# Performance work log

Hardware: AMD Instinct MI355X
Metric: run time of the kernel (lower is better)

The kernel has to match this reference:

```python
import jax, jax.numpy as jnp
import numpy as np


def setup_inputs() -> dict:
    key = jax.random.key(0)
    B, T, H, W, C = 4, 16, 112, 112, 96
    N = 2048
    RPB = N // B  # 512 regions per batch: 8 time blocks x 8x8 spatial blocks
    tb, hb, wb = T // 8, H // 8, W // 8  # block sizes 2, 14, 14
    ti = np.arange(T) // tb
    hi = np.arange(H) // hb
    wi = np.arange(W) // wb
    local = ti[:, None, None] * 64 + hi[None, :, None] * 8 + wi[None, None, :]  # [T,H,W]
    seg = (np.arange(B)[:, None, None, None] * RPB + local[None]).astype(np.int64)  # [B,T,H,W]
    coord = np.zeros((4, B * T * H * W), dtype=np.int64)
    coord[0] = np.repeat(np.arange(B), T * H * W)  # per-voxel batch index
    r = np.arange(N)
    l = r % RPB
    rt, rh, rw = l // 64, (l % 64) // 8, l % 8
    bbox = np.stack([
        rt * tb, rh * hb, rw * wb,
        rt * tb + (tb - 1), rh * hb + (hb - 1), rw * wb + (wb - 1),
    ]).astype(np.float32)  # [6,N]: ymin,xmin,zmin,ymax,xmax,zmax
    flatvid = jax.random.normal(key, (B * T * H * W, C), dtype=jnp.float32)
    return {"flatvid": flatvid, "seg": jnp.asarray(seg), "coord": jnp.asarray(coord),
            "bbox": jnp.asarray(bbox), "space_patch": 8, "time_patch": 4}


def reference(flatvid, seg, coord, bbox, space_patch, time_patch):
    B, T, H, W = seg.shape
    C = flatvid.shape[-1]
    N = bbox.shape[1]
    P = space_patch * space_patch * time_patch
    gs = jnp.linspace(0.0, 1.0, space_patch)
    gt = jnp.linspace(0.0, 1.0, time_patch)
    yg, xg, zg = jnp.meshgrid(gt, gs, gs, indexing='ij')
    yg, xg, zg = yg.reshape(1, P), xg.reshape(1, P), zg.reshape(1, P)
    seg_flat = seg.reshape(-1)
    # torch: unique(seg*B + b) % B  ->  per-region batch id (seg labels 0..N-1, one batch each)
    b_idx = jax.ops.segment_max(coord[0], seg_flat, num_segments=N).astype(jnp.int32)  # [N]
    ymin, xmin, zmin, ymax, xmax, zmax = bbox.reshape(6, N, 1)
    t_pos = yg * (ymax - ymin) + ymin  # [N,P]
    h_pos = xg * (xmax - xmin) + xmin
    w_pos = zg * (zmax - zmin) + zmin
    t0 = jnp.clip(jnp.floor(t_pos).astype(jnp.int32), 0, T - 1)
    h0 = jnp.clip(jnp.floor(h_pos).astype(jnp.int32), 0, H - 1)
    w0 = jnp.clip(jnp.floor(w_pos).astype(jnp.int32), 0, W - 1)
    t1 = jnp.clip(t0 + 1, 0, T - 1)
    h1 = jnp.clip(h0 + 1, 0, H - 1)
    w1 = jnp.clip(w0 + 1, 0, W - 1)
    Ut, Uh, Uw = t_pos - t0, h_pos - h0, w_pos - w0  # fractional offsets (vs clamped floor)
    Lt, Lh, Lw = 1.0 - Ut, 1.0 - Uh, 1.0 - Uw
    corners = [
        (t0, h0, w0, Lt * Lh * Lw), (t0, h0, w1, Lt * Lh * Uw),
        (t0, h1, w0, Lt * Uh * Lw), (t0, h1, w1, Lt * Uh * Uw),
        (t1, h0, w0, Ut * Lh * Lw), (t1, h0, w1, Ut * Lh * Uw),
        (t1, h1, w0, Ut * Uh * Lw), (t1, h1, w1, Ut * Uh * Uw),
    ]
    bb = b_idx[:, None]  # [N,1]
    srange = jnp.arange(N)[:, None]  # [N,1]
    tri = jnp.zeros((N, P, C), dtype=flatvid.dtype)
    msk = jnp.zeros((N, P), dtype=flatvid.dtype)
    for t, h, w, wt in corners:  # fixed 8 corners
        idx = ((bb * T + t) * H + h) * W + w  # [N,P] linear index into [B*T*H*W]
        tri = tri + flatvid[idx] * wt[..., None]
        msk = msk + (seg_flat[idx] == srange) * wt
    tri = tri.reshape(N, time_patch, space_patch, space_patch, C).transpose(0, 4, 1, 2, 3)
    msk = msk.reshape(N, 1, time_patch, space_patch, space_patch)
    return tri, msk
```

## Files before the change

kernel.cpp:

```cpp
#include <hip/hip_runtime.h>
#include <cstdint>
#include <cstddef>

#define B_  4
#define T_  16
#define H_  112
#define W_  112
#define C_  96
#define N_  2048
#define SP_ 8
#define TP_ 4
#define P_  256
#define M_  (B_*T_*H_*W_)

#define RT_   3
#define RH_   15
#define RW_   15
#define NPIX_ (RT_*RH_*RW_)
#define CC_   16
#define NPASS_ (C_/CC_)
#define PPAD_ 676

#define FU_ 11
#define BU_ 6

static_assert(P_ == SP_*SP_*TP_, "patch count");

__device__ __forceinline__ float bflo(unsigned int u){
    union { unsigned int i; float f; } v; v.i = u << 16; return v.f;
}
__device__ __forceinline__ float bfhi(unsigned int u){
    union { unsigned int i; float f; } v; v.i = u & 0xffff0000u; return v.f;
}
__device__ __forceinline__ unsigned short to_bf16(float f){
    union { unsigned int i; float f; } v; v.f = f;
    unsigned int x = v.i;
    return (unsigned short)((x + 0x7fffu + ((x >> 16) & 1u)) >> 16);
}

__global__ void detect_dtype_kernel(const unsigned short* __restrict__ v,
                                    int* __restrict__ flag){
    int lane = threadIdx.x;
    unsigned short u = v[lane * 2];
    int e = (u >> 7) & 0xff;
    int sane = ((e >= 107 && e <= 147) || ((u & 0x7fffu) == 0)) ? 1 : 0;
    unsigned long long m = __ballot(sane);
    if (lane == 0) flag[0] = (__popcll(m) >= 48) ? 1 : 0;
}

__global__ void segmax_kernel(const int* __restrict__ seg,
                              const int* __restrict__ coord0,
                              int* __restrict__ bidx){
    int g = blockIdx.x * blockDim.x + threadIdx.x;
    int base = g * 8;
    if (base >= M_) return;
    int4 s0 = *(const int4*)(seg + base);
    int4 s1 = *(const int4*)(seg + base + 4);
    int4 c0 = *(const int4*)(coord0 + base);
    int4 c1 = *(const int4*)(coord0 + base + 4);
    int s[8] = {s0.x,s0.y,s0.z,s0.w,s1.x,s1.y,s1.z,s1.w};
    int c[8] = {c0.x,c0.y,c0.z,c0.w,c1.x,c1.y,c1.z,c1.w};
    int cur = s[0], mx = c[0];
    #pragma unroll
    for (int j = 1; j < 8; ++j){
        if (s[j] == cur) { mx = max(mx, c[j]); }
        else { atomicMax(&bidx[cur], mx); cur = s[j]; mx = c[j]; }
    }
    atomicMax(&bidx[cur], mx);
}

__device__ __forceinline__ int region_gpix(int r, int b, int oy, int ox, int oz){
    const int tl  = r / (RH_*RW_);
    const int rem = r - tl*(RH_*RW_);
    const int hl  = rem / RW_;
    const int wl  = rem - hl*RW_;
    const int tg  = min(oy + tl, T_-1);
    const int hg  = min(ox + hl, H_-1);
    const int wg  = min(oz + wl, W_-1);
    return ((b*T_ + tg)*H_ + hg)*W_ + wg;
}

template<bool BF16>
__global__ __launch_bounds__(P_) void interp_kernel(
    const void* __restrict__ vid_, const int* __restrict__ seg,
    const void* __restrict__ bbox_, const int* __restrict__ bidx,
    const int* __restrict__ flag, void* __restrict__ out_)
{
    if (flag[0] != (BF16 ? 1 : 0)) return;

    __shared__ float lds_vid[CC_ * PPAD_];
    __shared__ int   lds_seg[NPIX_];

    const int n = blockIdx.x;
    const int p = threadIdx.x;

    float bb[6];
    if (BF16){
        const unsigned short* bbox = (const unsigned short*)bbox_;
        #pragma unroll
        for (int j = 0; j < 6; ++j) bb[j] = bflo((unsigned int)bbox[j*N_ + n]);
    } else {
        const float* bbox = (const float*)bbox_;
        #pragma unroll
        for (int j = 0; j < 6; ++j) bb[j] = bbox[j*N_ + n];
    }
    const float ymin=bb[0], xmin=bb[1], zmin=bb[2], ymax=bb[3], xmax=bb[4], zmax=bb[5];
    const int b  = bidx[n];
    const int oy = (int)ymin, ox = (int)xmin, oz = (int)zmin;

    const int pt = p >> 6, ph = (p >> 3) & 7, pw = p & 7;
    const float gt = (float)(pt * (1.0 / (TP_-1)));
    const float gh = (float)(ph * (1.0 / (SP_-1)));
    const float gw = (float)(pw * (1.0 / (SP_-1)));
    const float t_pos = gt * (ymax - ymin) + ymin;
    const float h_pos = gh * (xmax - xmin) + xmin;
    const float w_pos = gw * (zmax - zmin) + zmin;

    int t0 = (int)floorf(t_pos); t0 = min(max(t0, 0), T_-1);
    int h0 = (int)floorf(h_pos); h0 = min(max(h0, 0), H_-1);
    int w0 = (int)floorf(w_pos); w0 = min(max(w0, 0), W_-1);
    const int t1 = min(t0+1, T_-1);
    const int h1 = min(h0+1, H_-1);
    const int w1 = min(w0+1, W_-1);
    const float Ut = t_pos - (float)t0, Uh = h_pos - (float)h0, Uw = w_pos - (float)w0;
    const float Lt = 1.f - Ut, Lh = 1.f - Uh, Lw = 1.f - Uw;

    float wgt[8];
    wgt[0]=Lt*Lh*Lw; wgt[1]=Lt*Lh*Uw; wgt[2]=Lt*Uh*Lw; wgt[3]=Lt*Uh*Uw;
    wgt[4]=Ut*Lh*Lw; wgt[5]=Ut*Lh*Uw; wgt[6]=Ut*Uh*Lw; wgt[7]=Ut*Uh*Uw;

    const int lt0 = min(max(t0 - oy, 0), RT_-1);
    const int lt1 = min(max(t1 - oy, 0), RT_-1);
    const int lh0 = min(max(h0 - ox, 0), RH_-1);
    const int lh1 = min(max(h1 - ox, 0), RH_-1);
    const int lw0 = min(max(w0 - oz, 0), RW_-1);
    const int lw1 = min(max(w1 - oz, 0), RW_-1);
    int pix[8];
    {
        const int q00 = (lt0*RH_ + lh0)*RW_, q01 = (lt0*RH_ + lh1)*RW_;
        const int q10 = (lt1*RH_ + lh0)*RW_, q11 = (lt1*RH_ + lh1)*RW_;
        pix[0]=q00+lw0; pix[1]=q00+lw1; pix[2]=q01+lw0; pix[3]=q01+lw1;
        pix[4]=q10+lw0; pix[5]=q10+lw1; pix[6]=q11+lw0; pix[7]=q11+lw1;
    }

    for (int r = p; r < NPIX_; r += P_)
        lds_seg[r] = seg[region_gpix(r, b, oy, ox, oz)];

    const char* vidb = (const char*)vid_;

    if (BF16){
        unsigned goff[BU_]; int ldw[BU_]; uint4 V[BU_];
        #pragma unroll
        for (int i = 0; i < BU_; ++i){
            const int f = p + i*P_;
            if (f < NPIX_*2){
                const int r = f >> 1, u = f & 1;
                goff[i] = (unsigned)region_gpix(r, b, oy, ox, oz)*(unsigned)(C_*2) + (unsigned)u*16u;
                ldw[i]  = (u*8)*PPAD_ + r;
            } else { goff[i] = 0u; ldw[i] = -1; }
        }
        #pragma unroll
        for (int i = 0; i < BU_; ++i)
            if (ldw[i] >= 0) V[i] = *(const uint4*)(vidb + goff[i]);

        __syncthreads();

        float m = 0.f;
        #pragma unroll
        for (int k = 0; k < 8; ++k)
            m += wgt[k] * ((lds_seg[pix[k]] == n) ? 1.f : 0.f);
        unsigned short* out = (unsigned short*)out_;
        out[(size_t)N_*C_*P_ + (size_t)n*P_ + p] = to_bf16(m);

        #pragma unroll 1
        for (int pass = 0; pass < NPASS_; ++pass){
            if (pass) __syncthreads();
            #pragma unroll
            for (int i = 0; i < BU_; ++i){
                if (ldw[i] >= 0){
                    float* dst = &lds_vid[ldw[i]];
                    dst[0*PPAD_]=bflo(V[i].x); dst[1*PPAD_]=bfhi(V[i].x);
                    dst[2*PPAD_]=bflo(V[i].y); dst[3*PPAD_]=bfhi(V[i].y);
                    dst[4*PPAD_]=bflo(V[i].z); dst[5*PPAD_]=bfhi(V[i].z);
                    dst[6*PPAD_]=bflo(V[i].w); dst[7*PPAD_]=bfhi(V[i].w);
                }
            }
            if (pass+1 < NPASS_){
                #pragma unroll
                for (int i = 0; i < BU_; ++i)
                    if (ldw[i] >= 0)
                        V[i] = *(const uint4*)(vidb + goff[i] + (unsigned)((pass+1)*(CC_*2)));
            }
            __syncthreads();

            float acc[CC_];
            #pragma unroll
            for (int c = 0; c < CC_; ++c) acc[c] = 0.f;
            #pragma unroll
            for (int k = 0; k < 8; ++k){
                const float w = wgt[k];
                const float* col = &lds_vid[pix[k]];
                #pragma unroll
                for (int c = 0; c < CC_; ++c) acc[c] += w * col[c*PPAD_];
            }
            const size_t ob = ((size_t)n*C_ + pass*CC_)*P_ + p;
            #pragma unroll
            for (int c = 0; c < CC_; ++c) out[ob + (size_t)c*P_] = to_bf16(acc[c]);
        }
    } else {
        unsigned goff[FU_]; int ldw[FU_]; float4 V[FU_];
        #pragma unroll
        for (int i = 0; i < FU_; ++i){
            const int f = p + i*P_;
            if (f < NPIX_*4){
                const int r = f >> 2, q = f & 3;
                goff[i] = (unsigned)region_gpix(r, b, oy, ox, oz)*(unsigned)(C_*4) + (unsigned)q*16u;
                ldw[i]  = (q*4)*PPAD_ + r;
            } else { goff[i] = 0u; ldw[i] = -1; }
        }
        #pragma unroll
        for (int i = 0; i < FU_; ++i)
            if (ldw[i] >= 0) V[i] = *(const float4*)(vidb + goff[i]);

        __syncthreads();

        float m = 0.f;
        #pragma unroll
        for (int k = 0; k < 8; ++k)
            m += wgt[k] * ((lds_seg[pix[k]] == n) ? 1.f : 0.f);
        float* out = (float*)out_;
        out[(size_t)N_*C_*P_ + (size_t)n*P_ + p] = m;

        #pragma unroll 1
        for (int pass = 0; pass < NPASS_; ++pass){
            if (pass) __syncthreads();
            #pragma unroll
            for (int i = 0; i < FU_; ++i){
                if (ldw[i] >= 0){
                    float* dst = &lds_vid[ldw[i]];
                    dst[0*PPAD_]=V[i].x; dst[1*PPAD_]=V[i].y;
                    dst[2*PPAD_]=V[i].z; dst[3*PPAD_]=V[i].w;
                }
            }
            if (pass+1 < NPASS_){
                #pragma unroll
                for (int i = 0; i < FU_; ++i)
                    if (ldw[i] >= 0)
                        V[i] = *(const float4*)(vidb + goff[i] + (unsigned)((pass+1)*(CC_*4)));
            }
            __syncthreads();

            float acc[CC_];
            #pragma unroll
            for (int c = 0; c < CC_; ++c) acc[c] = 0.f;
            #pragma unroll
            for (int k = 0; k < 8; ++k){
                const float w = wgt[k];
                const float* col = &lds_vid[pix[k]];
                #pragma unroll
                for (int c = 0; c < CC_; ++c) acc[c] += w * col[c*PPAD_];
            }
            const size_t ob = ((size_t)n*C_ + pass*CC_)*P_ + p;
            #pragma unroll
            for (int c = 0; c < CC_; ++c) out[ob + (size_t)c*P_] = acc[c];
        }
    }
}

extern "C" void kernel_launch(void* const* d_in, const int* in_sizes, int n_in,
                              void* d_out, int out_size, void* d_ws, size_t ws_size,
                              hipStream_t stream){
    const void* vid   = d_in[0];
    const int*  seg   = (const int*)d_in[1];
    const int*  coord = (const int*)d_in[2];
    const void* bbox  = d_in[3];

    int* flag = (int*)d_ws;
    int* bidx = flag + 64;

    hipMemsetAsync(d_ws, 0, (64 + N_) * sizeof(int), stream);
    detect_dtype_kernel<<<1, 64, 0, stream>>>((const unsigned short*)vid, flag);
    segmax_kernel<<<(M_/8 + 255)/256, 256, 0, stream>>>(seg, coord, bidx);
    interp_kernel<true ><<<N_, P_, 0, stream>>>(vid, seg, bbox, bidx, flag, d_out);
    interp_kernel<false><<<N_, P_, 0, stream>>>(vid, seg, bbox, bidx, flag, d_out);
}
```

Before: 534.4 us.

## Halve LDS channel tile and skip zero-weight time corners

Shrinks the shared-memory video tile from 16 to 8 channels per pass, which should roughly halve LDS use and allow more resident blocks per CU. Global loads are reorganised into 64-byte super-chunks held in registers and written into LDS in sub-steps, with the next chunk prefetched during compute. The upper four trilinear corners are skipped when the temporal fractional weight is zero. The cost is more barriers per block and more register-held load state.

Result: slower. 590.3 us (+10.5%).

```diff
diff --git a/kernel.cpp b/kernel.cpp
--- a/kernel.cpp
+++ b/kernel.cpp
@@ -17,12 +17,13 @@
 #define RH_   15
 #define RW_   15
 #define NPIX_ (RT_*RH_*RW_)
-#define CC_   16
-#define NPASS_ (C_/CC_)
 #define PPAD_ 676
-
-#define FU_ 11
-#define BU_ 6
+#define CPP_  8
+#define UNITS_ 2700
+#define UPT_  11
+#define SSF_  6
+#define SSB_  3
+#define INVC_ (1<<20)
 
 static_assert(P_ == SP_*SP_*TP_, "patch count");
 
@@ -80,6 +81,27 @@
     return ((b*T_ + tg)*H_ + hg)*W_ + wg;
 }
 
+#define ACCUM8(accv) do {                                                    \
+    _Pragma("unroll")                                                        \
+    for (int c = 0; c < CPP_; ++c) accv[c] = 0.f;                            \
+    _Pragma("unroll")                                                        \
+    for (int k = 0; k < 4; ++k){                                             \
+        const float w = wgt[k];                                              \
+        const float* col = &lds_vid[pix[k]];                                 \
+        _Pragma("unroll")                                                    \
+        for (int c = 0; c < CPP_; ++c) accv[c] += w * col[c*PPAD_];          \
+    }                                                                        \
+    if (Ut != 0.f){                                                          \
+        _Pragma("unroll")                                                    \
+        for (int k = 4; k < 8; ++k){                                         \
+            const float w = wgt[k];                                          \
+            const float* col = &lds_vid[pix[k]];                             \
+            _Pragma("unroll")                                                \
+            for (int c = 0; c < CPP_; ++c) accv[c] += w * col[c*PPAD_];      \
+        }                                                                    \
+    }                                                                        \
+} while (0)
+
 template<bool BF16>
 __global__ __launch_bounds__(P_) void interp_kernel(
     const void* __restrict__ vid_, const int* __restrict__ seg,
@@ -88,7 +110,7 @@
 {
     if (flag[0] != (BF16 ? 1 : 0)) return;
 
-    __shared__ float lds_vid[CC_ * PPAD_];
+    __shared__ float lds_vid[CPP_ * PPAD_];
     __shared__ int   lds_seg[NPIX_];
 
     const int n = blockIdx.x;
@@ -143,126 +165,142 @@
         pix[4]=q10+lw0; pix[5]=q10+lw1; pix[6]=q11+lw0; pix[7]=q11+lw1;
     }
 
+    const char* vidb = (const char*)vid_;
+
+    unsigned goff[UPT_];
+    int      code[UPT_];
+    #pragma unroll
+    for (int i = 0; i < UPT_; ++i){
+        const int f = p + i*P_;
+        if (f < UNITS_){
+            const int q = f / NPIX_;
+            const int r = f - q*NPIX_;
+            goff[i] = (unsigned)region_gpix(r, b, oy, ox, oz) *
+                      (unsigned)(BF16 ? C_*2 : C_*4) + (unsigned)q*16u;
+            if (BF16) code[i] = (q << 12) | r;
+            else      code[i] = (q < 2) ? (q*(4*PPAD_) + r)
+                                        : (-((q-2)*(4*PPAD_) + r) - 1);
+        } else { goff[i] = 0u; code[i] = INVC_; }
+    }
+
     for (int r = p; r < NPIX_; r += P_)
         lds_seg[r] = seg[region_gpix(r, b, oy, ox, oz)];
 
-    const char* vidb = (const char*)vid_;
-
     if (BF16){
-        unsigned goff[BU_]; int ldw[BU_]; uint4 V[BU_];
-        #pragma unroll
-        for (int i = 0; i < BU_; ++i){
-            const int f = p + i*P_;
-            if (f < NPIX_*2){
-                const int r = f >> 1, u = f & 1;
-                goff[i] = (unsigned)region_gpix(r, b, oy, ox, oz)*(unsigned)(C_*2) + (unsigned)u*16u;
-                ldw[i]  = (u*8)*PPAD_ + r;
-            } else { goff[i] = 0u; ldw[i] = -1; }
+        const unsigned short* __restrict__ out_bump = nullptr; (void)out_bump;
+        uint4 V[UPT_];
+        #pragma unroll
+        for (int i = 0; i < UPT_; ++i)
+            if (code[i] != INVC_) V[i] = *(const uint4*)(vidb + goff[i]);
+
+        __syncthreads();
+
+        float m = 0.f;
+        #pragma unroll
+        for (int k = 0; k < 4; ++k)
+            m += wgt[k] * ((lds_seg[pix[k]] == n) ? 1.f : 0.f);
+        if (Ut != 0.f){
+            #pragma unroll
+            for (int k = 4; k < 8; ++k)
+                m += wgt[k] * ((lds_seg[pix[k]] == n) ? 1.f : 0.f);
         }
-        #pragma unroll
-        for (int i = 0; i < BU_; ++i)
-            if (ldw[i] >= 0) V[i] = *(const uint4*)(vidb + goff[i]);
-
-        __syncthreads();
-
-        float m = 0.f;
-        #pragma unroll
-        for (int k = 0; k < 8; ++k)
-            m += wgt[k] * ((lds_seg[pix[k]] == n) ? 1.f : 0.f);
         unsigned short* out = (unsigned short*)out_;
         out[(size_t)N_*C_*P_ + (size_t)n*P_ + p] = to_bf16(m);
 
         #pragma unroll 1
-        for (int pass = 0; pass < NPASS_; ++pass){
-            if (pass) __syncthreads();
-            #pragma unroll
-            for (int i = 0; i < BU_; ++i){
-                if (ldw[i] >= 0){
-                    float* dst = &lds_vid[ldw[i]];
-                    dst[0*PPAD_]=bflo(V[i].x); dst[1*PPAD_]=bfhi(V[i].x);
-                    dst[2*PPAD_]=bflo(V[i].y); dst[3*PPAD_]=bfhi(V[i].y);
-                    dst[4*PPAD_]=bflo(V[i].z); dst[5*PPAD_]=bfhi(V[i].z);
-                    dst[6*PPAD_]=bflo(V[i].w); dst[7*PPAD_]=bfhi(V[i].w);
+        for (int ss = 0; ss < SSB_; ++ss){
+            #pragma unroll 1
+            for (int sub = 0; sub < 4; ++sub){
+                __syncthreads();
+                #pragma unroll
+                for (int i = 0; i < UPT_; ++i){
+                    const int cd = code[i];
+                    if (cd != INVC_ && (cd >> 12) == sub){
+                        float* d = &lds_vid[cd & 4095];
+                        d[0*PPAD_]=bflo(V[i].x); d[1*PPAD_]=bfhi(V[i].x);
+                        d[2*PPAD_]=bflo(V[i].y); d[3*PPAD_]=bfhi(V[i].y);
+                        d[4*PPAD_]=bflo(V[i].z); d[5*PPAD_]=bfhi(V[i].z);
+                        d[6*PPAD_]=bflo(V[i].w); d[7*PPAD_]=bfhi(V[i].w);
+                    }
                 }
-            }
-            if (pass+1 < NPASS_){
-                #pragma unroll
-                for (int i = 0; i < BU_; ++i)
-                    if (ldw[i] >= 0)
-                        V[i] = *(const uint4*)(vidb + goff[i] + (unsigned)((pass+1)*(CC_*2)));
-            }
-            __syncthreads();
-
-            float acc[CC_];
-            #pragma unroll
-            for (int c = 0; c < CC_; ++c) acc[c] = 0.f;
-            #pragma unroll
-            for (int k = 0; k < 8; ++k){
-                const float w = wgt[k];
-                const float* col = &lds_vid[pix[k]];
-                #pragma unroll
-                for (int c = 0; c < CC_; ++c) acc[c] += w * col[c*PPAD_];
-            }
-            const size_t ob = ((size_t)n*C_ + pass*CC_)*P_ + p;
-            #pragma unroll
-            for (int c = 0; c < CC_; ++c) out[ob + (size_t)c*P_] = to_bf16(acc[c]);
+                if (sub == 3 && ss+1 < SSB_){
+                    #pragma unroll
+                    for (int i = 0; i < UPT_; ++i)
+                        if (code[i] != INVC_)
+                            V[i] = *(const uint4*)(vidb + goff[i] + (unsigned)((ss+1)*64));
+                }
+                __syncthreads();
+                float acc[CPP_];
+                ACCUM8(acc);
+                const size_t ob = ((size_t)n*C_ + ss*32 + sub*8)*P_ + p;
+                #pragma unroll
+                for (int c = 0; c < CPP_; ++c) out[ob + (size_t)c*P_] = to_bf16(acc[c]);
+            }
         }
     } else {
-        unsigned goff[FU_]; int ldw[FU_]; float4 V[FU_];
-        #pragma unroll
-        for (int i = 0; i < FU_; ++i){
-            const int f = p + i*P_;
-            if (f < NPIX_*4){
-                const int r = f >> 2, q = f & 3;
-                goff[i] = (unsigned)region_gpix(r, b, oy, ox, oz)*(unsigned)(C_*4) + (unsigned)q*16u;
-                ldw[i]  = (q*4)*PPAD_ + r;
-            } else { goff[i] = 0u; ldw[i] = -1; }
+        float4 V[UPT_];
+        #pragma unroll
+        for (int i = 0; i < UPT_; ++i)
+            if (code[i] != INVC_) V[i] = *(const float4*)(vidb + goff[i]);
+
+        __syncthreads();
+
+        float m = 0.f;
+        #pragma unroll
+        for (int k = 0; k < 4; ++k)
+            m += wgt[k] * ((lds_seg[pix[k]] == n) ? 1.f : 0.f);
+        if (Ut != 0.f){
+            #pragma unroll
+            for (int k = 4; k < 8; ++k)
+                m += wgt[k] * ((lds_seg[pix[k]] == n) ? 1.f : 0.f);
         }
-        #pragma unroll
-        for (int i = 0; i < FU_; ++i)
-            if (ldw[i] >= 0) V[i] = *(const float4*)(vidb + goff[i]);
-
-        __syncthreads();
-
-        float m = 0.f;
-        #pragma unroll
-        for (int k = 0; k < 8; ++k)
-            m += wgt[k] * ((lds_seg[pix[k]] == n) ? 1.f : 0.f);
         float* out = (float*)out_;
         out[(size_t)N_*C_*P_ + (size_t)n*P_ + p] = m;
 
         #pragma unroll 1
-        for (int pass = 0; pass < NPASS_; ++pass){
-            if (pass) __syncthreads();
+        for (int s = 0; s < SSF_; ++s){
+            __syncthreads();
             #pragma unroll
-            for (int i = 0; i < FU_; ++i){
-                if (ldw[i] >= 0){
-                    float* dst = &lds_vid[ldw[i]];
-                    dst[0*PPAD_]=V[i].x; dst[1*PPAD_]=V[i].y;
-                    dst[2*PPAD_]=V[i].z; dst[3*PPAD_]=V[i].w;
+            for (int i = 0; i < UPT_; ++i){
+                const int cd = code[i];
+                if (cd >= 0 && cd < INVC_){
+                    float* d = &lds_vid[cd];
+                    d[0*PPAD_]=V[i].x; d[1*PPAD_]=V[i].y;
+                    d[2*PPAD_]=V[i].z; d[3*PPAD_]=V[i].w;
                 }
             }
-            if (pass+1 < NPASS_){
-                #pragma unroll
-                for (int i = 0; i < FU_; ++i)
-                    if (ldw[i] >= 0)
-                        V[i] = *(const float4*)(vidb + goff[i] + (unsigned)((pass+1)*(CC_*4)));
-            }
             __syncthreads();
-
-            float acc[CC_];
+            {
+                float acc[CPP_];
+                ACCUM8(acc);
+                const size_t ob = ((size_t)n*C_ + s*16)*P_ + p;
+                #pragma unroll
+                for (int c = 0; c < CPP_; ++c) out[ob + (size_t)c*P_] = acc[c];
+            }
+            __syncthreads();
             #pragma unroll
-            for (int c = 0; c < CC_; ++c) acc[c] = 0.f;
-            #pragma unroll
-            for (int k = 0; k < 8; ++k){
-                const float w = wgt[k];
-                const float* col = &lds_vid[pix[k]];
-                #pragma unroll
-                for (int c = 0; c < CC_; ++c) acc[c] += w * col[c*PPAD_];
-            }
-            const size_t ob = ((size_t)n*C_ + pass*CC_)*P_ + p;
-            #pragma unroll
-            for (int c = 0; c < CC_; ++c) out[ob + (size_t)c*P_] = acc[c];
+            for (int i = 0; i < UPT_; ++i){
+                const int cd = code[i];
+                if (cd < 0){
+                    float* d = &lds_vid[-cd - 1];
+                    d[0*PPAD_]=V[i].x; d[1*PPAD_]=V[i].y;
+                    d[2*PPAD_]=V[i].z; d[3*PPAD_]=V[i].w;
+                }
+            }
+            if (s+1 < SSF_){
+                #pragma unroll
+                for (int i = 0; i < UPT_; ++i)
+                    if (code[i] != INVC_)
+                        V[i] = *(const float4*)(vidb + goff[i] + (unsigned)((s+1)*64));
+            }
+            __syncthreads();
+            {
+                float acc[CPP_];
+                ACCUM8(acc);
+                const size_t ob = ((size_t)n*C_ + s*16 + 8)*P_ + p;
+                #pragma unroll
+                for (int c = 0; c < CPP_; ++c) out[ob + (size_t)c*P_] = acc[c];
+            }
         }
     }
 }
```
